# Optimization experiments

Hardware: AMD Instinct MI355X
Metric: run time of the kernel (lower is better)

The kernel has to match this reference:

```python
import jax, jax.numpy as jnp
import numpy as np
from jax import lax

EPS = 1e-5

@jax.custom_vjp
def bin_active(x):
    # forward: sign binarization (original also returns channel-mean of |x|, which is discarded)
    return jnp.sign(x)

def _ba_fwd(x):
    return jnp.sign(x), x

def _ba_bwd(x, g):
    # straight-through estimator: zero grad where |x| >= 1
    return (jnp.where((x >= 1.0) | (x <= -1.0), 0.0, g),)

bin_active.defvjp(_ba_fwd, _ba_bwd)


def setup_inputs() -> dict:
    key = jax.random.key(0)
    k1, k2 = jax.random.split(key)
    N, C_in, H, W_sp = 64, 256, 56, 56
    C_out, K = 256, 3
    x = jax.random.normal(k1, (N, C_in, H, W_sp), dtype=jnp.float32)
    gamma = jnp.ones((C_in,), dtype=jnp.float32)
    beta = jnp.zeros((C_in,), dtype=jnp.float32)
    W = jax.random.normal(k2, (C_out, C_in, K, K), dtype=jnp.float32) * 0.05
    return {"x": x, "gamma": gamma, "beta": beta, "W": W}


def reference(x, gamma, beta, W):
    # BatchNorm2d (training-mode batch stats), affine
    mean = jnp.mean(x, axis=(0, 2, 3), keepdims=True)          # [1,C,1,1]
    var = jnp.var(x, axis=(0, 2, 3), keepdims=True)
    xn = (x - mean) * lax.rsqrt(var + EPS)
    xn = xn * gamma.reshape(1, -1, 1, 1) + beta.reshape(1, -1, 1, 1)
    # binarize activations
    xb = bin_active(xn)
    # Conv2d stride=1 pad=1, no bias, then ReLU
    y = lax.conv_general_dilated(
        xb, W,
        window_strides=(1, 1),
        padding=[(1, 1), (1, 1)],
        dimension_numbers=("NCHW", "OIHW", "NCHW"),
    )
    return jax.nn.relu(y)
```

## Files before the change

kernel.cpp:

```cpp
#include <hip/hip_runtime.h>
#include <hip/hip_bf16.h>
#include <stdint.h>

#define HP 58
#define WP 64
#define CIN 256
#define COUT 256
#define HH 56
#define WW 56
#define IMG_STRIDE (HP*WP*CIN)
#define ROW_STRIDE (WP*CIN)
#define NPIX 200704.0

#define XO    2048
#define XROW  14848
#define AO    93184
#define LDS_TOTAL 142336

typedef __attribute__((ext_vector_type(4))) int i32x4;

#define GLDS(g, l) __builtin_amdgcn_global_load_lds( \
    (const __attribute__((address_space(1))) void*)(g), \
    (__attribute__((address_space(3))) void*)(l), 16, 0, 0)

__global__ __launch_bounds__(256) void stats_partial(const float* __restrict__ x,
                                                     double* __restrict__ part) {
  int b = blockIdx.x;
  int c = b >> 6, n = b & 63;
  const float4* p = (const float4*)(x + (size_t)(n*CIN + c) * (HH*WW));
  double s = 0.0, s2 = 0.0;
  for (int i = threadIdx.x; i < 784; i += 256) {
    float4 v = p[i];
    double a0 = v.x, a1 = v.y, a2 = v.z, a3 = v.w;
    s  += (a0 + a1) + (a2 + a3);
    s2 += (a0*a0 + a1*a1) + (a2*a2 + a3*a3);
  }
  for (int off = 32; off > 0; off >>= 1) {
    s  += __shfl_down(s, off);
    s2 += __shfl_down(s2, off);
  }
  __shared__ double red[8];
  int wv = threadIdx.x >> 6, ln = threadIdx.x & 63;
  if (ln == 0) { red[wv*2] = s; red[wv*2+1] = s2; }
  __syncthreads();
  if (threadIdx.x == 0) {
    double ts = ((red[0]+red[2])+red[4])+red[6];
    double t2 = ((red[1]+red[3])+red[5])+red[7];
    part[(size_t)(c*64 + n)*2]     = ts;
    part[(size_t)(c*64 + n)*2 + 1] = t2;
  }
}

__global__ void stats_final(const double* __restrict__ part,
                            const float* __restrict__ gamma,
                            const float* __restrict__ beta,
                            double* __restrict__ prm) {
  int c = threadIdx.x;
  double s = 0.0, s2 = 0.0;
  for (int n = 0; n < 64; ++n) {
    s  += part[(size_t)(c*64+n)*2];
    s2 += part[(size_t)(c*64+n)*2 + 1];
  }
  double mean = s / NPIX;
  double var  = s2 / NPIX - mean*mean;
  double inv  = 1.0 / sqrt(var + 1e-5);
  prm[c*4+0] = mean;
  prm[c*4+1] = (double)gamma[c] * inv;
  prm[c*4+2] = (double)beta[c];
}

__global__ __launch_bounds__(256) void binarize(const float* __restrict__ x,
                                                const double* __restrict__ prm,
                                                int8_t* __restrict__ xb) {
  int b = blockIdx.x;
  int n = b / HP, y = b % HP;
  int8_t* orow = xb + (size_t)(n*HP + y) * ROW_STRIDE;
  if (y == 0 || y == HP-1) {
    int4 z = {0,0,0,0};
    int4* q = (int4*)orow;
    for (int i = threadIdx.x; i < ROW_STRIDE/16; i += 256) q[i] = z;
    return;
  }
  __shared__ char sbuf[WW][260];
  int h  = y - 1;
  int tid = threadIdx.x;
  #pragma unroll
  for (int it = 0; it < 14; ++it) {
    int t = it*256 + tid;
    int c = t / 14, j = t - c*14;
    float4 v = *(const float4*)(x + (size_t)(n*CIN + c)*(HH*WW) + h*WW + j*4);
    double mu = prm[c*4], gi = prm[c*4+1], be = prm[c*4+2];
    #pragma unroll
    for (int e = 0; e < 4; ++e) {
      double xv = (double)((&v.x)[e]);
      double vv = (xv - mu)*gi + be;
      sbuf[j*4+e][c] = vv > 0.0 ? (int8_t)1 : (vv < 0.0 ? (int8_t)-1 : (int8_t)0);
    }
  }
  __syncthreads();
  int xh = tid >> 6, cq = tid & 63;
  uint32_t* orow32 = (uint32_t*)orow;
  for (int xx0 = 0; xx0 < WP; xx0 += 4) {
    int xx = xx0 + xh;
    uint32_t v = 0;
    if (xx >= 1 && xx <= WW) v = *(const uint32_t*)&sbuf[xx-1][cq*4];
    orow32[xx*64 + cq] = v;
  }
}

__global__ __launch_bounds__(256) void wrepack(const float* __restrict__ W,
                                               int8_t* __restrict__ Wb,
                                               float* __restrict__ invs) {
  int co = blockIdx.x, ci = threadIdx.x;
  float w[9]; float mx = 0.f;
  const float* p = W + (size_t)co*(CIN*9) + ci*9;
  #pragma unroll
  for (int t = 0; t < 9; ++t) { w[t] = p[t]; mx = fmaxf(mx, fabsf(w[t])); }
  for (int off = 32; off > 0; off >>= 1) mx = fmaxf(mx, __shfl_xor(mx, off));
  __shared__ float sm[4];
  if ((threadIdx.x & 63) == 0) sm[threadIdx.x >> 6] = mx;
  __syncthreads();
  mx = fmaxf(fmaxf(sm[0], sm[1]), fmaxf(sm[2], sm[3]));
  float s = mx > 0.f ? 127.f / mx : 0.f;
  #pragma unroll
  for (int t = 0; t < 9; ++t) {
    int q = (int)lrintf(w[t] * s);
    q = q > 127 ? 127 : (q < -127 ? -127 : q);
    Wb[t*(COUT*CIN) + co*CIN + ci] = (int8_t)q;
  }
  if (threadIdx.x == 0) invs[co] = mx / 127.f;
}

__global__ __launch_bounds__(512, 2) void conv_gemm(const int8_t* __restrict__ xb,
                                                    const int8_t* __restrict__ Wb,
                                                    const float* __restrict__ invs,
                                                    float* __restrict__ out) {
  extern __shared__ char smem[];
  int bid = blockIdx.x;
  int swz = (bid & 7) * 112 + (bid >> 3);
  int n_img = swz / 14, rg = swz - n_img * 14;
  int y0 = 1 + rg * 4;

  int tid = threadIdx.x;
  int ln = tid & 63, wid = tid >> 6;
  int wm = wid >> 2, wn = wid & 3;

  size_t xoff = (size_t)n_img * IMG_STRIDE + (size_t)(y0 - 1) * ROW_STRIDE;

  #pragma unroll
  for (int i = 0; i < 11; ++i) {
    int o = tid*16 + i*8192;
    if (o < 89088) {
      int r   = o / XROW;
      int rem = o - r*XROW;
      int xx  = rem >> 8, cb = rem & 255;
      const int8_t* src = xb + xoff + r*ROW_STRIDE + xx*256 + (cb ^ ((xx & 7) << 4));
      GLDS(src, smem + XO + o);
    }
  }

  int arow = tid & 255, aslice = tid >> 8;
  auto STAGE_A = [&](int s, int buf) {
    int sc = s < 36 ? s : 35;
    int tap = sc >> 2, ci0 = (sc & 3) << 6;
    const int8_t* base = Wb + tap*(COUT*CIN) + arow*256 + ci0;
    char* dst = smem + AO + buf*16384 + tid*16;
    GLDS(base + aslice*16,       dst);
    GLDS(base + (2+aslice)*16,   dst + 8192);
  };

  i32x4 acc[8][4] = {};
  STAGE_A(0, 0); STAGE_A(1, 1);

  int afrag = ((ln >> 4) << 12) + (wm*128 + (ln & 15)) * 16;
  int xx0   = ln & 15;
  int cb16  = (ln >> 4) << 4;
  int bufr = 0, bufs = 2;

  #pragma unroll 1
  for (int s = 0; s < 36; ++s) {
    asm volatile("s_waitcnt vmcnt(2)" ::: "memory");
    __builtin_amdgcn_s_barrier();
    STAGE_A(s + 2, bufs);

    int tap = s >> 2, ci0q = (s & 3) << 6;
    int kh = (tap * 11) >> 5;
    int kw = tap - kh * 3;

    i32x4 a[8], b[4];
    const char* Ab = smem + AO + bufr*16384 + afrag;
    #pragma unroll
    for (int m = 0; m < 8; ++m) a[m] = *(const i32x4*)(Ab + m*256);
    int cb = ci0q + cb16;
    const char* Xr = smem + XO + (wn + kh) * XROW;
    #pragma unroll
    for (int nn = 0; nn < 4; ++nn) {
      int x_in = xx0 + nn*16 + kw - 1;
      b[nn] = *(const i32x4*)(Xr + x_in*256 + (cb ^ ((x_in & 7) << 4)));
    }

    asm volatile("s_waitcnt lgkmcnt(0)" ::: "memory");
    __builtin_amdgcn_sched_barrier(0);
    __builtin_amdgcn_s_setprio(1);
    #pragma unroll
    for (int m = 0; m < 8; ++m)
      #pragma unroll
      for (int nn = 0; nn < 4; ++nn)
        acc[m][nn] = __builtin_amdgcn_mfma_i32_16x16x64_i8(a[m], b[nn], acc[m][nn], 0, 0, 0);
    __builtin_amdgcn_s_setprio(0);

    bufr = bufr == 2 ? 0 : bufr + 1;
    bufs = bufs == 2 ? 0 : bufs + 1;
  }

  asm volatile("s_waitcnt vmcnt(0)" ::: "memory");
  __syncthreads();

  float ivv[8][4];
  #pragma unroll
  for (int m = 0; m < 8; ++m)
    #pragma unroll
    for (int r = 0; r < 4; ++r)
      ivv[m][r] = invs[wm*128 + m*16 + (ln >> 4)*4 + r];

  char* eb = smem + wid * 16384;
  int y = y0 + wn;
  size_t obase = (size_t)n_img * COUT * (HH*WW) + (size_t)(y - 1) * WW;

  #pragma unroll
  for (int p = 0; p < 2; ++p) {
    #pragma unroll
    for (int m2 = 0; m2 < 4; ++m2) {
      int m = p*4 + m2;
      #pragma unroll
      for (int nn = 0; nn < 4; ++nn)
        #pragma unroll
        for (int r = 0; r < 4; ++r) {
          int row  = m2*16 + (ln >> 4)*4 + r;
          int slot = (nn*16 + (ln & 15) + 63) & 63;
          float v = fmaxf((float)acc[m][nn][r] * ivv[m][r], 0.0f);
          *(float*)(eb + row*256 + ((slot*4) ^ ((row & 7) << 5))) = v;
        }
    }
    asm volatile("s_waitcnt lgkmcnt(0)" ::: "memory");
    __builtin_amdgcn_s_barrier();
    int co = wm*128 + p*64 + ln;
    const char* rbase = eb + ln*256;
    float* op = out + obase + (size_t)co * (HH*WW);
    #pragma unroll
    for (int j = 0; j < 14; ++j) {
      float4 v = *(const float4*)(rbase + ((j*16) ^ ((ln & 7) << 5)));
      *(float4*)(op + j*4) = v;
    }
    asm volatile("s_waitcnt lgkmcnt(0)" ::: "memory");
    __builtin_amdgcn_s_barrier();
  }
}

extern "C" void kernel_launch(void* const* d_in, const int* in_sizes, int n_in,
                              void* d_out, int out_size, void* d_ws, size_t ws_size,
                              hipStream_t stream) {
  const float* x     = (const float*)d_in[0];
  const float* gamma = (const float*)d_in[1];
  const float* beta  = (const float*)d_in[2];
  const float* W     = (const float*)d_in[3];
  float* out = (float*)d_out;

  char* ws = (char*)d_ws;
  double*  part = (double*)ws;
  double*  prm  = (double*)(ws + 262144);
  float*   invs = (float*)(ws + 270336);
  int8_t*  Wb   = (int8_t*)(ws + 271360);
  int8_t*  xbuf = (int8_t*)(ws + 1048576);

  (void)hipFuncSetAttribute((const void*)conv_gemm,
                            hipFuncAttributeMaxDynamicSharedMemorySize, LDS_TOTAL);

  hipLaunchKernelGGL(wrepack,       dim3(256),    dim3(256), 0, stream, W, Wb, invs);
  hipLaunchKernelGGL(stats_partial, dim3(256*64), dim3(256), 0, stream, x, part);
  hipLaunchKernelGGL(stats_final,   dim3(1),      dim3(256), 0, stream, part, gamma, beta, prm);
  hipLaunchKernelGGL(binarize,      dim3(64*HP),  dim3(256), 0, stream, x, prm, xbuf);
  hipLaunchKernelGGL(conv_gemm,     dim3(896),    dim3(512), LDS_TOTAL, stream, xbuf, Wb, invs, out);
}
```

Baseline: 321.2 us.

## Deepen weight staging to four buffers, prefetch LDS fragments, and coalesce epilogue stores

The weight tile staging ring grows from three to four LDS buffers, prefetched three steps ahead. LDS fragment reads for step s+1 are now issued before the MFMAs of step s, using double-buffered registers, so the explicit lgkmcnt wait and sched barrier are gone. The epilogue changes its swizzle so that 16 lanes write one output row as contiguous float4 stores, and it drops the intra-wave barriers. In exchange the kernel uses more LDS and more registers, which may reduce occupancy.

```diff
diff --git a/kernel.cpp b/kernel.cpp
--- a/kernel.cpp
+++ b/kernel.cpp
@@ -15,7 +15,7 @@
 #define XO    2048
 #define XROW  14848
 #define AO    93184
-#define LDS_TOTAL 142336
+#define LDS_TOTAL 158720
 
 typedef __attribute__((ext_vector_type(4))) int i32x4;
 
@@ -170,47 +170,52 @@
   };
 
   i32x4 acc[8][4] = {};
-  STAGE_A(0, 0); STAGE_A(1, 1);
+  STAGE_A(0, 0); STAGE_A(1, 1); STAGE_A(2, 2);
 
   int afrag = ((ln >> 4) << 12) + (wm*128 + (ln & 15)) * 16;
   int xx0   = ln & 15;
   int cb16  = (ln >> 4) << 4;
-  int bufr = 0, bufs = 2;
-
-  #pragma unroll 1
-  for (int s = 0; s < 36; ++s) {
+
+  i32x4 aR[2][8], bR[2][4];
+
+  auto LOADF = [&](int s, i32x4 (&av)[8], i32x4 (&bv)[4]) {
+    int sc = s < 36 ? s : 35;
+    const char* Ab = smem + AO + (s & 3)*16384 + afrag;
+    #pragma unroll
+    for (int m = 0; m < 8; ++m) av[m] = *(const i32x4*)(Ab + m*256);
+    int tap = sc >> 2;
+    int kh = (tap * 11) >> 5, kw = tap - kh * 3;
+    int cb = ((sc & 3) << 6) + cb16;
+    const char* Xr = smem + XO + (wn + kh) * XROW;
+    #pragma unroll
+    for (int nn = 0; nn < 4; ++nn) {
+      int x_in = xx0 + nn*16 + kw - 1;
+      bv[nn] = *(const i32x4*)(Xr + x_in*256 + (cb ^ ((x_in & 7) << 4)));
+    }
+  };
+
+  asm volatile("s_waitcnt vmcnt(4)" ::: "memory");
+  __builtin_amdgcn_s_barrier();
+  LOADF(0, aR[0], bR[0]);
+
+  auto body = [&](int s, i32x4 (&ac)[8], i32x4 (&bc)[4], i32x4 (&an)[8], i32x4 (&bn)[4]) {
     asm volatile("s_waitcnt vmcnt(2)" ::: "memory");
     __builtin_amdgcn_s_barrier();
-    STAGE_A(s + 2, bufs);
-
-    int tap = s >> 2, ci0q = (s & 3) << 6;
-    int kh = (tap * 11) >> 5;
-    int kw = tap - kh * 3;
-
-    i32x4 a[8], b[4];
-    const char* Ab = smem + AO + bufr*16384 + afrag;
-    #pragma unroll
-    for (int m = 0; m < 8; ++m) a[m] = *(const i32x4*)(Ab + m*256);
-    int cb = ci0q + cb16;
-    const char* Xr = smem + XO + (wn + kh) * XROW;
-    #pragma unroll
-    for (int nn = 0; nn < 4; ++nn) {
-      int x_in = xx0 + nn*16 + kw - 1;
-      b[nn] = *(const i32x4*)(Xr + x_in*256 + (cb ^ ((x_in & 7) << 4)));
-    }
-
-    asm volatile("s_waitcnt lgkmcnt(0)" ::: "memory");
-    __builtin_amdgcn_sched_barrier(0);
+    STAGE_A(s + 3, (s + 3) & 3);
+    LOADF(s + 1, an, bn);
     __builtin_amdgcn_s_setprio(1);
     #pragma unroll
     for (int m = 0; m < 8; ++m)
       #pragma unroll
       for (int nn = 0; nn < 4; ++nn)
-        acc[m][nn] = __builtin_amdgcn_mfma_i32_16x16x64_i8(a[m], b[nn], acc[m][nn], 0, 0, 0);
+        acc[m][nn] = __builtin_amdgcn_mfma_i32_16x16x64_i8(ac[m], bc[nn], acc[m][nn], 0, 0, 0);
     __builtin_amdgcn_s_setprio(0);
-
-    bufr = bufr == 2 ? 0 : bufr + 1;
-    bufs = bufs == 2 ? 0 : bufs + 1;
+  };
+
+  #pragma unroll 1
+  for (int t = 0; t < 18; ++t) {
+    body(2*t,     aR[0], bR[0], aR[1], bR[1]);
+    body(2*t + 1, aR[1], bR[1], aR[0], bR[0]);
   }
 
   asm volatile("s_waitcnt vmcnt(0)" ::: "memory");
@@ -238,22 +243,22 @@
         for (int r = 0; r < 4; ++r) {
           int row  = m2*16 + (ln >> 4)*4 + r;
           int slot = (nn*16 + (ln & 15) + 63) & 63;
+          int q    = (row >> 2) & 3;
           float v = fmaxf((float)acc[m][nn][r] * ivv[m][r], 0.0f);
-          *(float*)(eb + row*256 + ((slot*4) ^ ((row & 7) << 5))) = v;
+          *(float*)(eb + row*256 + (((slot ^ (q << 4))) << 2)) = v;
         }
     }
-    asm volatile("s_waitcnt lgkmcnt(0)" ::: "memory");
-    __builtin_amdgcn_s_barrier();
-    int co = wm*128 + p*64 + ln;
-    const char* rbase = eb + ln*256;
-    float* op = out + obase + (size_t)co * (HH*WW);
-    #pragma unroll
-    for (int j = 0; j < 14; ++j) {
-      float4 v = *(const float4*)(rbase + ((j*16) ^ ((ln & 7) << 5)));
-      *(float4*)(op + j*4) = v;
-    }
-    asm volatile("s_waitcnt lgkmcnt(0)" ::: "memory");
-    __builtin_amdgcn_s_barrier();
+    int c16 = ln & 15, rq = ln >> 4;
+    #pragma unroll
+    for (int j = 0; j < 16; ++j) {
+      int row = j*4 + rq;
+      int q   = (row >> 2) & 3;
+      float4 v = *(const float4*)(eb + row*256 + ((c16 << 4) ^ (q << 6)));
+      if (c16 < 14) {
+        int co = wm*128 + p*64 + row;
+        *(float4*)(out + obase + (size_t)co*(HH*WW) + c16*4) = v;
+      }
+    }
   }
 }
 
```

New measurement: 281.9 us. 1.14x faster.
